# Kernel tuning notes

Measured on AMD Instinct MI355X. Metric: run time of the kernel, lower is better.

Reference implementation:

```python
import jax, jax.numpy as jnp
import numpy as np
from jax import lax

DN = ('NCHW', 'OIHW', 'NCHW')

def _conv(x, w, pad):
    return lax.conv_general_dilated(x, w, (1, 1), [(pad, pad), (pad, pad)], dimension_numbers=DN)

def _bn(x, g, b, eps=1e-5):
    # BatchNorm2d in training mode: batch statistics over (N,H,W), biased variance
    m = jnp.mean(x, axis=(0, 2, 3), keepdims=True)
    v = jnp.var(x, axis=(0, 2, 3), keepdims=True)
    return (x - m) * lax.rsqrt(v + eps) * g.reshape(1, -1, 1, 1) + b.reshape(1, -1, 1, 1)

def setup_inputs() -> dict:
    key = jax.random.key(0)
    ks = jax.random.split(key, 24)
    B, H, W = 128, 64, 64
    l_i, lh = 2, (150, 120, 100)
    l_q, cf = 10, H * W
    r = lambda k, s, sc: jax.random.normal(k, s, dtype=jnp.float32) * sc
    return {
        'X': r(ks[0], (B, l_i, H, W), 1.0),
        'obs': r(ks[1], (B, 24), 1.0),
        'h1_w': r(ks[2], (lh[0], l_i, 3, 3), 0.1), 'h1_b': r(ks[3], (lh[0],), 0.05),
        'g1': jnp.ones((lh[0],), jnp.float32), 'b1': jnp.zeros((lh[0],), jnp.float32),
        'h2_w': r(ks[4], (lh[1], lh[0], 3, 3), 0.03), 'h2_b': r(ks[5], (lh[1],), 0.05),
        'g2': jnp.ones((lh[1],), jnp.float32), 'b2': jnp.zeros((lh[1],), jnp.float32),
        'h3_w': r(ks[6], (lh[2], lh[1], 3, 3), 0.03), 'h3_b': r(ks[7], (lh[2],), 0.05),
        'g3': jnp.ones((lh[2],), jnp.float32), 'b3': jnp.zeros((lh[2],), jnp.float32),
        'r_w': r(ks[8], (1, lh[2], 1, 1), 0.1),
        'q_w': r(ks[9], (l_q, 1, 5, 5), 0.1),
        'w': r(ks[10], (l_q, 1, 5, 5), 0.05),  # Parameter (zeros init in torch; randn here for nontrivial math)
        'fc1_w': r(ks[11], (100, 24), 0.1), 'fc1_b': r(ks[12], (100,), 0.05),
        'fc2_w': r(ks[13], (10, 100), 0.1), 'fc2_b': r(ks[14], (10,), 0.05),
        'cv_w': r(ks[15], (1, cf), 0.02), 'cv_b': r(ks[16], (1,), 0.05),
        'K': 36,
    }

def reference(X, obs, h1_w, h1_b, g1, b1, h2_w, h2_b, g2, b2, h3_w, h3_b, g3, b3,
              r_w, q_w, w, fc1_w, fc1_b, fc2_w, fc2_b, cv_w, cv_b, K):
    relu = jax.nn.relu
    h = relu(_bn(_conv(X, h1_w, 1) + h1_b.reshape(1, -1, 1, 1), g1, b1))
    h = relu(_bn(_conv(h, h2_w, 1) + h2_b.reshape(1, -1, 1, 1), g2, b2))
    h = relu(_bn(_conv(h, h3_w, 1) + h3_b.reshape(1, -1, 1, 1), g3, b3))
    r = _conv(h, r_w, 0)                      # [B,1,H,W] reward map
    qr = _conv(r, q_w, 2)                     # conv of r part is constant across VI iterations
    v = jnp.max(qr, axis=1, keepdims=True)    # [B,1,H,W]
    # conv2d(cat([r,v],1), cat([q_w,w],1)) == conv(r,q_w) + conv(v,w)
    def step(v, _):
        q = qr + _conv(v, w, 2)
        return jnp.max(q, axis=1, keepdims=True), None
    # original: K-1 loop iterations + 1 extra conv/max = K total steps after the init
    v, _ = lax.scan(step, v, None, length=K)
    critic = v.reshape(v.shape[0], -1) @ cv_w.T + cv_b
    action_pred = relu(relu(obs @ fc1_w.T + fc1_b) @ fc2_w.T + fc2_b)
    return (critic, action_pred)
```

## Files before the change

### kernel.cpp

```cpp
#include <hip/hip_runtime.h>


#define NHW 524288.0f

typedef __attribute__((ext_vector_type(8))) short v8s;
typedef __attribute__((ext_vector_type(4))) float v4f;

static __device__ __forceinline__ float bf2f(unsigned short u) {
  return __uint_as_float(((unsigned int)u) << 16);
}
static __device__ __forceinline__ unsigned short f2bf(float f) {
  unsigned int x = __float_as_uint(f);
  return (unsigned short)((x + 0x7fffu + ((x >> 16) & 1u)) >> 16);
}
static __device__ __forceinline__ float wave_sum(float s) {
  #pragma unroll
  for (int off = 32; off > 0; off >>= 1) s += __shfl_down(s, off, 64);
  return s;
}

template <int CO, int CI, int CIP>
__global__ __launch_bounds__(256) void repack_w(
    const float* __restrict__ w, unsigned short* __restrict__ Wp)
{
  int i = blockIdx.x * 256 + threadIdx.x;
  const int total = 9 * 128 * CIP;
  if (i >= total) return;
  int pos = i / (128 * CIP);
  int rem = i - pos * (128 * CIP);
  int co  = rem / CIP;
  int ci  = rem - co * CIP;
  float v = (co < CO && ci < CI) ? w[(co * CI + ci) * 9 + pos] : 0.f;
  Wp[i] = f2bf(v);
}

__global__ __launch_bounds__(256) void conv1_stats(
    const float* __restrict__ X, const float* __restrict__ w1,
    const float* __restrict__ b1, float* __restrict__ S, float* __restrict__ Q)
{
  const int tile = blockIdx.x;
  const int b    = tile >> 3;
  const int y0t  = (tile & 7) * 8;
  const int co0  = blockIdx.y * 15;
  const int tid  = threadIdx.x;
  const int x    = tid & 63;
  const int ly0  = (tid >> 6) * 2;

  __shared__ float lin[2][10][66];
  __shared__ float ss[15], qq[15];
  if (tid < 15) { ss[tid] = 0.f; qq[tid] = 0.f; }
  for (int idx = tid; idx < 2 * 10 * 66; idx += 256) {
    int cc = idx / 660, rem = idx - cc * 660;
    int rr = rem / 66,  c   = rem - rr * 66;
    int yy = y0t + rr - 1, xx = c - 1;
    lin[cc][rr][c] = (yy >= 0 && yy < 64 && xx >= 0 && xx < 64)
                         ? X[((size_t)(b * 2 + cc) << 12) + (yy << 6) + xx] : 0.f;
  }
  __syncthreads();

  float iv[2][4][3];
  #pragma unroll
  for (int cc = 0; cc < 2; cc++)
    #pragma unroll
    for (int r = 0; r < 4; r++)
      #pragma unroll
      for (int c = 0; c < 3; c++) iv[cc][r][c] = lin[cc][ly0 + r][x + c];

  #pragma unroll
  for (int co = 0; co < 15; co++) {
    const float* w9 = w1 + (size_t)(co0 + co) * 18;
    float a0 = 0.f, a1 = 0.f;
    #pragma unroll
    for (int cc = 0; cc < 2; cc++)
      #pragma unroll
      for (int ky = 0; ky < 3; ky++)
        #pragma unroll
        for (int kx = 0; kx < 3; kx++) {
          float wv = w9[cc * 9 + ky * 3 + kx];
          a0 = fmaf(iv[cc][ky][kx],     wv, a0);
          a1 = fmaf(iv[cc][ky + 1][kx], wv, a1);
        }
    float bz = b1[co0 + co];
    float t0 = a0 + bz, t1 = a1 + bz;
    float s  = wave_sum(t0 + t1);
    float q  = wave_sum(t0 * t0 + t1 * t1);
    if ((tid & 63) == 0) { atomicAdd(&ss[co], s); atomicAdd(&qq[co], q); }
  }
  __syncthreads();
  if (tid < 15) {
    atomicAdd(&S[co0 + tid], ss[tid]);
    atomicAdd(&Q[co0 + tid], qq[tid]);
  }
}

template <int C>
__global__ void bn_finalize(const float* __restrict__ S, const float* __restrict__ Q,
                            const float* __restrict__ g, const float* __restrict__ be,
                            float* __restrict__ A, float* __restrict__ Bs)
{
  int c = threadIdx.x;
  if (c < C) {
    const float invN = 1.f / NHW;
    float m   = S[c] * invN;
    float var = fmaxf(Q[c] * invN - m * m, 0.f);
    float sc  = g[c] * rsqrtf(var + 1e-5f);
    A[c]  = sc;
    Bs[c] = be[c] - m * sc;
  }
}

__global__ __launch_bounds__(256, 2) void conv2_mfma(
    const float* __restrict__ X,  const float* __restrict__ w1,
    const float* __restrict__ b1f, const float* __restrict__ A1,
    const float* __restrict__ B1, const unsigned short* __restrict__ W2p,
    const float* __restrict__ b2, unsigned short* __restrict__ t2)
{
  const int bx   = blockIdx.x;
  const int b    = bx >> 4;
  const int t16  = bx & 15;
  const int y0   = (t16 >> 2) * 16;
  const int x0   = (t16 & 3) * 16;
  const int tid  = threadIdx.x;
  const int lane = tid & 63;
  const int wid  = __builtin_amdgcn_readfirstlane(tid >> 6);
  const int ln   = lane & 15;
  const int quad = (lane >> 4) * 8;

  __shared__ __align__(16) float Xs[2][20][20];
  __shared__ float w1s[2700];
  __shared__ float A1s[150], B1s[150], b1s[150], b2s[128];
  __shared__ __align__(16) unsigned short Atile[324 * 34];
  __shared__ __align__(16) unsigned short outs[256 * 68];

  for (int i = tid; i < 2700; i += 256) w1s[i] = w1[i];
  for (int i = tid; i < 150; i += 256) { A1s[i] = A1[i]; B1s[i] = B1[i]; b1s[i] = b1f[i]; }
  if (tid < 128) b2s[tid] = (tid < 120) ? b2[tid] : 0.f;
  for (int i = tid; i < 800; i += 256) {
    int c2 = i / 400, rem = i - c2 * 400;
    int rr = rem / 20, cc = rem - rr * 20;
    int gy = y0 - 2 + rr, gx = x0 - 2 + cc;
    Xs[c2][rr][cc] = (gy >= 0 && gy < 64 && gx >= 0 && gx < 64)
                         ? X[((size_t)(b * 2 + c2) << 12) + (gy << 6) + gx] : 0.f;
  }

  v4f acc[4][8];
  #pragma unroll
  for (int i = 0; i < 4; i++)
    #pragma unroll
    for (int j = 0; j < 8; j++) acc[i][j] = (v4f){0.f, 0.f, 0.f, 0.f};

  for (int chunk = 0; chunk < 5; chunk++) {
    __syncthreads();
    {
      const int ci_loc = tid & 31;
      const int ci = chunk * 32 + ci_loc;
      const bool live = (ci < 150);
      float wv[18], sc = 0.f, sh = 0.f, bz = 0.f;
      if (live) {
        #pragma unroll
        for (int k = 0; k < 18; k++) wv[k] = w1s[ci * 18 + k];
        sc = A1s[ci]; sh = B1s[ci]; bz = b1s[ci];
      }
      for (int pass = 0; pass < 41; pass++) {
        int p = pass * 8 + (tid >> 5);
        if (p < 324) {
          float v = 0.f;
          if (live) {
            int pr = p / 18, pc = p - pr * 18;
            int hy = y0 - 1 + pr, hx = x0 - 1 + pc;
            if (hy >= 0 && hy < 64 && hx >= 0 && hx < 64) {
              float a = bz;
              #pragma unroll
              for (int c2 = 0; c2 < 2; c2++)
                #pragma unroll
                for (int ky = 0; ky < 3; ky++)
                  #pragma unroll
                  for (int kx = 0; kx < 3; kx++)
                    a = fmaf(Xs[c2][pr + ky][pc + kx], wv[c2 * 9 + ky * 3 + kx], a);
              v = fmaxf(fmaf(a, sc, sh), 0.f);
            }
          }
          Atile[p * 34 + ci_loc] = f2bf(v);
        }
      }
    }
    __syncthreads();

    v8s afr[6][3];
    #pragma unroll
    for (int t = 0; t < 6; t++)
      #pragma unroll
      for (int kx = 0; kx < 3; kx++)
        afr[t][kx] = *(const v8s*)(&Atile[((wid * 4 + t) * 18 + ln + kx) * 34 + quad]);

    #pragma unroll
    for (int pos = 0; pos < 9; pos++) {
      const int ky = pos / 3, kx = pos - ky * 3;
      const unsigned short* bw =
          W2p + (size_t)(pos * 128 + ln) * 160 + chunk * 32 + quad;
      v8s bf[8];
      #pragma unroll
      for (int nj = 0; nj < 8; nj++)
        bf[nj] = *(const v8s*)(bw + (size_t)nj * 16 * 160);
      #pragma unroll
      for (int mi = 0; mi < 4; mi++) {
        #pragma unroll
        for (int nj = 0; nj < 8; nj++)
          acc[mi][nj] = __builtin_amdgcn_mfma_f32_16x16x32_bf16(
              afr[mi + ky][kx], bf[nj], acc[mi][nj], 0, 0, 0);
      }
    }
  }

  #pragma unroll
  for (int half = 0; half < 2; half++) {
    __syncthreads();
    #pragma unroll
    for (int mi = 0; mi < 4; mi++)
      #pragma unroll
      for (int njl = 0; njl < 4; njl++) {
        int n = njl * 16 + ln;
        float bz = b2s[half * 64 + n];
        #pragma unroll
        for (int r2 = 0; r2 < 4; r2++) {
          int m = wid * 64 + mi * 16 + (lane >> 4) * 4 + r2;
          outs[m * 68 + n] = f2bf(acc[mi][half * 4 + njl][r2] + bz);
        }
      }
    __syncthreads();
    const int ng = half ? 7 : 8;
    for (int i = tid; i < 256 * ng; i += 256) {
      int p = i / ng, g = i - p * ng;
      int gy = y0 + (p >> 4), gx = x0 + (p & 15);
      size_t gpx = ((size_t)b << 12) + (gy << 6) + gx;
      *(uint4*)(t2 + gpx * 120 + half * 64 + g * 8) =
          *(const uint4*)(&outs[p * 68 + g * 8]);
    }
  }
}

__global__ __launch_bounds__(256, 2) void conv3_mfma(
    const unsigned short* __restrict__ t2, const float* __restrict__ A2,
    const float* __restrict__ B2, const unsigned short* __restrict__ W3p,
    const float* __restrict__ b3, unsigned short* __restrict__ t3)
{
  const int bx   = blockIdx.x;
  const int b    = bx >> 4;
  const int t16  = bx & 15;
  const int y0   = (t16 >> 2) * 16;
  const int x0   = (t16 & 3) * 16;
  const int tid  = threadIdx.x;
  const int lane = tid & 63;
  const int wid  = __builtin_amdgcn_readfirstlane(tid >> 6);
  const int ln   = lane & 15;
  const int quad = (lane >> 4) * 8;

  __shared__ float A2s[120], B2s[120], b3s[128];
  __shared__ __align__(16) unsigned short Atile[324 * 34];
  __shared__ __align__(16) unsigned short outs[256 * 68];

  for (int i = tid; i < 120; i += 256) { A2s[i] = A2[i]; B2s[i] = B2[i]; }
  if (tid < 128) b3s[tid] = (tid < 100) ? b3[tid] : 0.f;

  v4f acc[4][8];
  #pragma unroll
  for (int i = 0; i < 4; i++)
    #pragma unroll
    for (int j = 0; j < 8; j++) acc[i][j] = (v4f){0.f, 0.f, 0.f, 0.f};

  for (int chunk = 0; chunk < 4; chunk++) {
    __syncthreads();
    {
      const int ci0 = chunk * 32;
      const int ngr = (chunk == 3) ? 3 : 4;
      for (int i = tid; i < 1296; i += 256) {
        int p = i >> 2, g = i & 3;
        int pr = p / 18, pc = p - pr * 18;
        int hy = y0 - 1 + pr, hx = x0 - 1 + pc;
        union { uint4 v; unsigned short u[8]; } ov;
        ov.v = (uint4){0, 0, 0, 0};
        if (g < ngr && hy >= 0 && hy < 64 && hx >= 0 && hx < 64) {
          size_t gpx = ((size_t)b << 12) + (hy << 6) + hx;
          union { uint4 v; unsigned short u[8]; } in;
          in.v = *(const uint4*)(t2 + gpx * 120 + ci0 + g * 8);
          #pragma unroll
          for (int j = 0; j < 8; j++) {
            int ci = ci0 + g * 8 + j;
            ov.u[j] = f2bf(fmaxf(fmaf(bf2f(in.u[j]), A2s[ci], B2s[ci]), 0.f));
          }
        }
        *(uint4*)(&Atile[p * 34 + g * 8]) = ov.v;
      }
    }
    __syncthreads();

    v8s afr[6][3];
    #pragma unroll
    for (int t = 0; t < 6; t++)
      #pragma unroll
      for (int kx = 0; kx < 3; kx++)
        afr[t][kx] = *(const v8s*)(&Atile[((wid * 4 + t) * 18 + ln + kx) * 34 + quad]);

    #pragma unroll
    for (int pos = 0; pos < 9; pos++) {
      const int ky = pos / 3, kx = pos - ky * 3;
      const unsigned short* bw =
          W3p + (size_t)(pos * 128 + ln) * 128 + chunk * 32 + quad;
      v8s bf[8];
      #pragma unroll
      for (int nj = 0; nj < 8; nj++)
        bf[nj] = *(const v8s*)(bw + (size_t)nj * 16 * 128);
      #pragma unroll
      for (int mi = 0; mi < 4; mi++) {
        #pragma unroll
        for (int nj = 0; nj < 8; nj++)
          acc[mi][nj] = __builtin_amdgcn_mfma_f32_16x16x32_bf16(
              afr[mi + ky][kx], bf[nj], acc[mi][nj], 0, 0, 0);
      }
    }
  }

  #pragma unroll
  for (int half = 0; half < 2; half++) {
    __syncthreads();
    #pragma unroll
    for (int mi = 0; mi < 4; mi++)
      #pragma unroll
      for (int njl = 0; njl < 4; njl++) {
        int n = njl * 16 + ln;
        float bz = b3s[half * 64 + n];
        #pragma unroll
        for (int r2 = 0; r2 < 4; r2++) {
          int m = wid * 64 + mi * 16 + (lane >> 4) * 4 + r2;
          outs[m * 68 + n] = f2bf(acc[mi][half * 4 + njl][r2] + bz);
        }
      }
    __syncthreads();
    const int ng = half ? 5 : 8;
    for (int i = tid; i < 256 * ng; i += 256) {
      int p = i / ng, g = i - p * ng;
      int gy = y0 + (p >> 4), gx = x0 + (p & 15);
      size_t gpx = ((size_t)b << 12) + (gy << 6) + gx;
      *(uint4*)(t3 + gpx * 104 + half * 64 + g * 8) =
          *(const uint4*)(&outs[p * 68 + g * 8]);
    }
  }
}

template <int ST, int NG, int C>
__global__ __launch_bounds__(256) void nhwc_stats(
    const unsigned short* __restrict__ t, float* __restrict__ S, float* __restrict__ Q)
{
  const int tid = threadIdx.x;
  const int g   = tid & 15;
  const int pl  = tid >> 4;
  const bool valid = (g < NG);
  const int px0 = blockIdx.x * 512;

  __shared__ float ss[128], qq[128];
  for (int i = tid; i < 128; i += 256) { ss[i] = 0.f; qq[i] = 0.f; }
  __syncthreads();

  float s8[8], q8[8];
  #pragma unroll
  for (int j = 0; j < 8; j++) { s8[j] = 0.f; q8[j] = 0.f; }

  if (valid) {
    for (int it = 0; it < 32; it++) {
      size_t px = px0 + it * 16 + pl;
      union { uint4 v; unsigned short u[8]; } in;
      in.v = *(const uint4*)(t + px * ST + g * 8);
      #pragma unroll
      for (int j = 0; j < 8; j++) {
        float v = bf2f(in.u[j]);
        s8[j] += v;
        q8[j] += v * v;
      }
    }
    #pragma unroll
    for (int j = 0; j < 8; j++) {
      atomicAdd(&ss[g * 8 + j], s8[j]);
      atomicAdd(&qq[g * 8 + j], q8[j]);
    }
  }
  __syncthreads();
  if (tid < C) {
    atomicAdd(&S[tid], ss[tid]);
    atomicAdd(&Q[tid], qq[tid]);
  }
}

__global__ __launch_bounds__(256) void bn3_reduce_r(
    const unsigned short* __restrict__ t3, const float* __restrict__ A3,
    const float* __restrict__ B3, const float* __restrict__ rw,
    float* __restrict__ r)
{
  __shared__ float A3s[104], B3s[104], rws[104];
  const int tid = threadIdx.x;
  for (int i = tid; i < 104; i += 256) {
    bool v = (i < 100);
    A3s[i] = v ? A3[i] : 0.f;
    B3s[i] = v ? B3[i] : 0.f;
    rws[i] = v ? rw[i] : 0.f;
  }
  __syncthreads();

  size_t px = (size_t)blockIdx.x * 256 + tid;
  const unsigned short* p = t3 + px * 104;
  float a = 0.f;
  #pragma unroll
  for (int gq = 0; gq < 13; gq++) {
    union { uint4 v; unsigned short u[8]; } in;
    in.v = *(const uint4*)(p + gq * 8);
    #pragma unroll
    for (int j = 0; j < 8; j++) {
      int ci = gq * 8 + j;
      a = fmaf(fmaxf(fmaf(bf2f(in.u[j]), A3s[ci], B3s[ci]), 0.f), rws[ci], a);
    }
  }
  r[px] = a;
}

__global__ __launch_bounds__(256) void qr_init(
    const float* __restrict__ r, const float* __restrict__ qw,
    float* __restrict__ qr, float* __restrict__ v0)
{
  const int tile = blockIdx.x;
  const int b    = tile >> 4;
  const int y0t  = (tile & 15) * 4;
  const int tid  = threadIdx.x;
  const int x    = tid & 63;
  const int ly   = tid >> 6;

  __shared__ float lv[8][68];
  for (int idx = tid; idx < 8 * 68; idx += 256) {
    int rr = idx / 68, c = idx - rr * 68;
    int yy = y0t + rr - 2, xx = c - 2;
    lv[rr][c] = (yy >= 0 && yy < 64 && xx >= 0 && xx < 64)
                    ? r[((size_t)b << 12) + (yy << 6) + xx] : 0.f;
  }
  __syncthreads();

  float iv[5][5];
  #pragma unroll
  for (int ky = 0; ky < 5; ky++)
    #pragma unroll
    for (int kx = 0; kx < 5; kx++) iv[ky][kx] = lv[ly + ky][x + kx];

  const int y = y0t + ly;
  float vmax = -1e30f;
  #pragma unroll
  for (int a = 0; a < 10; a++) {
    float q = 0.f;
    #pragma unroll
    for (int ky = 0; ky < 5; ky++)
      #pragma unroll
      for (int kx = 0; kx < 5; kx++)
        q = fmaf(iv[ky][kx], qw[a * 25 + ky * 5 + kx], q);
    qr[((size_t)(b * 10 + a) << 12) + (y << 6) + x] = q;
    vmax = fmaxf(vmax, q);
  }
  v0[((size_t)b << 12) + (y << 6) + x] = vmax;
}

__global__ __launch_bounds__(256) void vi_step(
    const float* __restrict__ vin, const float* __restrict__ qr,
    const float* __restrict__ ww, float* __restrict__ vout)
{
  const int tile = blockIdx.x;
  const int b    = tile >> 4;
  const int y0t  = (tile & 15) * 4;
  const int tid  = threadIdx.x;
  const int x    = tid & 63;
  const int ly   = tid >> 6;

  __shared__ float lv[8][68];
  for (int idx = tid; idx < 8 * 68; idx += 256) {
    int rr = idx / 68, c = idx - rr * 68;
    int yy = y0t + rr - 2, xx = c - 2;
    lv[rr][c] = (yy >= 0 && yy < 64 && xx >= 0 && xx < 64)
                    ? vin[((size_t)b << 12) + (yy << 6) + xx] : 0.f;
  }
  __syncthreads();

  float iv[5][5];
  #pragma unroll
  for (int ky = 0; ky < 5; ky++)
    #pragma unroll
    for (int kx = 0; kx < 5; kx++) iv[ky][kx] = lv[ly + ky][x + kx];

  const int y = y0t + ly;
  float vmax = -1e30f;
  #pragma unroll
  for (int a = 0; a < 10; a++) {
    float q = qr[((size_t)(b * 10 + a) << 12) + (y << 6) + x];
    #pragma unroll
    for (int ky = 0; ky < 5; ky++)
      #pragma unroll
      for (int kx = 0; kx < 5; kx++)
        q = fmaf(iv[ky][kx], ww[a * 25 + ky * 5 + kx], q);
    vmax = fmaxf(vmax, q);
  }
  vout[((size_t)b << 12) + (y << 6) + x] = vmax;
}

__global__ __launch_bounds__(256) void critic_k(
    const float* __restrict__ v, const float* __restrict__ cvw,
    const float* __restrict__ cvb, float* __restrict__ out)
{
  const int b = blockIdx.x;
  const int tid = threadIdx.x;
  const float4* pv = (const float4*)(v + ((size_t)b << 12));
  const float4* pw = (const float4*)cvw;
  float s = 0.f;
  #pragma unroll
  for (int i = 0; i < 4; i++) {
    float4 a = pv[tid + 256 * i];
    float4 w = pw[tid + 256 * i];
    s += a.x * w.x + a.y * w.y + a.z * w.z + a.w * w.w;
  }
  s = wave_sum(s);
  __shared__ float ls[4];
  const int w = tid >> 6;
  if ((tid & 63) == 0) ls[w] = s;
  __syncthreads();
  if (tid == 0) out[b] = ls[0] + ls[1] + ls[2] + ls[3] + cvb[0];
}

__global__ __launch_bounds__(128) void action_k(
    const float* __restrict__ obs, const float* __restrict__ fc1w,
    const float* __restrict__ fc1b, const float* __restrict__ fc2w,
    const float* __restrict__ fc2b, float* __restrict__ out)
{
  const int b = blockIdx.x;
  const int j = threadIdx.x;
  __shared__ float ob[24];
  __shared__ float h[100];
  if (j < 24) ob[j] = obs[b * 24 + j];
  __syncthreads();
  if (j < 100) {
    float s = fc1b[j];
    #pragma unroll
    for (int k = 0; k < 24; k++) s = fmaf(ob[k], fc1w[j * 24 + k], s);
    h[j] = fmaxf(s, 0.f);
  }
  __syncthreads();
  if (j < 10) {
    float s = fc2b[j];
    for (int k = 0; k < 100; k++) s = fmaf(h[k], fc2w[j * 100 + k], s);
    out[128 + b * 10 + j] = fmaxf(s, 0.f);
  }
}

extern "C" void kernel_launch(void* const* d_in, const int* in_sizes, int n_in,
                              void* d_out, int out_size, void* d_ws,
                              size_t ws_size, hipStream_t stream)
{
  const float* X     = (const float*)d_in[0];
  const float* obs   = (const float*)d_in[1];
  const float* h1_w  = (const float*)d_in[2];
  const float* h1_b  = (const float*)d_in[3];
  const float* g1    = (const float*)d_in[4];
  const float* b1    = (const float*)d_in[5];
  const float* h2_w  = (const float*)d_in[6];
  const float* h2_b  = (const float*)d_in[7];
  const float* g2    = (const float*)d_in[8];
  const float* b2    = (const float*)d_in[9];
  const float* h3_w  = (const float*)d_in[10];
  const float* h3_b  = (const float*)d_in[11];
  const float* g3    = (const float*)d_in[12];
  const float* b3    = (const float*)d_in[13];
  const float* r_w   = (const float*)d_in[14];
  const float* q_w   = (const float*)d_in[15];
  const float* w_vi  = (const float*)d_in[16];
  const float* fc1_w = (const float*)d_in[17];
  const float* fc1_b = (const float*)d_in[18];
  const float* fc2_w = (const float*)d_in[19];
  const float* fc2_b = (const float*)d_in[20];
  const float* cv_w  = (const float*)d_in[21];
  const float* cv_b  = (const float*)d_in[22];

  char* ws = (char*)d_ws;
  unsigned short* t2  = (unsigned short*)ws;
  unsigned short* t3  = (unsigned short*)(ws + 125829120ull);
  unsigned short* W2p = (unsigned short*)(ws + 234881024ull);
  unsigned short* W3p = (unsigned short*)(ws + 235249664ull);
  float*          ST  = (float*)         (ws + 235544576ull);
  float* S1 = ST +    0; float* Q1 = ST +  150; float* A1 = ST +  300; float* B1 = ST +  450;
  float* S2 = ST +  600; float* Q2 = ST +  720; float* A2 = ST +  840; float* B2 = ST +  960;
  float* S3 = ST + 1080; float* Q3 = ST + 1180; float* A3 = ST + 1280; float* B3 = ST + 1380;
  float* r  = (float*)ws;
  float* qr = r + 524288;
  float* vA = qr + 5242880;
  float* vB = vA + 524288;

  hipMemsetAsync(ST, 0, 1480 * sizeof(float), stream);

  repack_w<120, 150, 160><<<720, 256, 0, stream>>>(h2_w, W2p);
  repack_w<100, 120, 128><<<576, 256, 0, stream>>>(h3_w, W3p);

  conv1_stats<<<dim3(1024, 10), 256, 0, stream>>>(X, h1_w, h1_b, S1, Q1);
  bn_finalize<150><<<1, 256, 0, stream>>>(S1, Q1, g1, b1, A1, B1);

  conv2_mfma<<<2048, 256, 0, stream>>>(X, h1_w, h1_b, A1, B1, W2p, h2_b, t2);
  nhwc_stats<120, 15, 120><<<1024, 256, 0, stream>>>(t2, S2, Q2);
  bn_finalize<120><<<1, 256, 0, stream>>>(S2, Q2, g2, b2, A2, B2);

  conv3_mfma<<<2048, 256, 0, stream>>>(t2, A2, B2, W3p, h3_b, t3);
  nhwc_stats<104, 13, 100><<<1024, 256, 0, stream>>>(t3, S3, Q3);
  bn_finalize<100><<<1, 256, 0, stream>>>(S3, Q3, g3, b3, A3, B3);

  bn3_reduce_r<<<2048, 256, 0, stream>>>(t3, A3, B3, r_w, r);

  qr_init<<<2048, 256, 0, stream>>>(r, q_w, qr, vA);
  for (int i = 0; i < 36; i++) {
    const float* vin = (i & 1) ? vB : vA;
    float* vout      = (i & 1) ? vA : vB;
    vi_step<<<2048, 256, 0, stream>>>(vin, qr, w_vi, vout);
  }

  float* out = (float*)d_out;
  critic_k<<<128, 256, 0, stream>>>(vA, cv_w, cv_b, out);
  action_k<<<128, 128, 0, stream>>>(obs, fc1_w, fc1_b, fc2_w, fc2_b, out);
}
```

Measured before the change: 1.319 ms.

## Fuse value-iteration loop and critic into one persistent per-image kernel

```diff
diff --git a/kernel.cpp b/kernel.cpp
--- a/kernel.cpp
+++ b/kernel.cpp
@@ -2,6 +2,7 @@
 
 
 #define NHW 524288.0f
+#define VSTR 69
 
 typedef __attribute__((ext_vector_type(8))) short v8s;
 typedef __attribute__((ext_vector_type(4))) float v4f;
@@ -421,110 +422,91 @@
   r[px] = a;
 }
 
-__global__ __launch_bounds__(256) void qr_init(
-    const float* __restrict__ r, const float* __restrict__ qw,
-    float* __restrict__ qr, float* __restrict__ v0)
-{
-  const int tile = blockIdx.x;
-  const int b    = tile >> 4;
-  const int y0t  = (tile & 15) * 4;
-  const int tid  = threadIdx.x;
-  const int x    = tid & 63;
-  const int ly   = tid >> 6;
-
-  __shared__ float lv[8][68];
-  for (int idx = tid; idx < 8 * 68; idx += 256) {
-    int rr = idx / 68, c = idx - rr * 68;
-    int yy = y0t + rr - 2, xx = c - 2;
-    lv[rr][c] = (yy >= 0 && yy < 64 && xx >= 0 && xx < 64)
-                    ? r[((size_t)b << 12) + (yy << 6) + xx] : 0.f;
-  }
-  __syncthreads();
-
-  float iv[5][5];
-  #pragma unroll
-  for (int ky = 0; ky < 5; ky++)
-    #pragma unroll
-    for (int kx = 0; kx < 5; kx++) iv[ky][kx] = lv[ly + ky][x + kx];
-
-  const int y = y0t + ly;
-  float vmax = -1e30f;
-  #pragma unroll
-  for (int a = 0; a < 10; a++) {
-    float q = 0.f;
-    #pragma unroll
-    for (int ky = 0; ky < 5; ky++)
-      #pragma unroll
-      for (int kx = 0; kx < 5; kx++)
-        q = fmaf(iv[ky][kx], qw[a * 25 + ky * 5 + kx], q);
-    qr[((size_t)(b * 10 + a) << 12) + (y << 6) + x] = q;
-    vmax = fmaxf(vmax, q);
-  }
-  v0[((size_t)b << 12) + (y << 6) + x] = vmax;
-}
-
-__global__ __launch_bounds__(256) void vi_step(
-    const float* __restrict__ vin, const float* __restrict__ qr,
-    const float* __restrict__ ww, float* __restrict__ vout)
-{
-  const int tile = blockIdx.x;
-  const int b    = tile >> 4;
-  const int y0t  = (tile & 15) * 4;
-  const int tid  = threadIdx.x;
-  const int x    = tid & 63;
-  const int ly   = tid >> 6;
-
-  __shared__ float lv[8][68];
-  for (int idx = tid; idx < 8 * 68; idx += 256) {
-    int rr = idx / 68, c = idx - rr * 68;
-    int yy = y0t + rr - 2, xx = c - 2;
-    lv[rr][c] = (yy >= 0 && yy < 64 && xx >= 0 && xx < 64)
-                    ? vin[((size_t)b << 12) + (yy << 6) + xx] : 0.f;
-  }
-  __syncthreads();
-
-  float iv[5][5];
-  #pragma unroll
-  for (int ky = 0; ky < 5; ky++)
-    #pragma unroll
-    for (int kx = 0; kx < 5; kx++) iv[ky][kx] = lv[ly + ky][x + kx];
-
-  const int y = y0t + ly;
-  float vmax = -1e30f;
-  #pragma unroll
-  for (int a = 0; a < 10; a++) {
-    float q = qr[((size_t)(b * 10 + a) << 12) + (y << 6) + x];
-    #pragma unroll
-    for (int ky = 0; ky < 5; ky++)
-      #pragma unroll
-      for (int kx = 0; kx < 5; kx++)
-        q = fmaf(iv[ky][kx], ww[a * 25 + ky * 5 + kx], q);
-    vmax = fmaxf(vmax, q);
-  }
-  vout[((size_t)b << 12) + (y << 6) + x] = vmax;
-}
-
-__global__ __launch_bounds__(256) void critic_k(
-    const float* __restrict__ v, const float* __restrict__ cvw,
+__global__ __launch_bounds__(512, 1) void vi_fused(
+    const float* __restrict__ r,   const float* __restrict__ qw,
+    const float* __restrict__ ww,  const float* __restrict__ cvw,
     const float* __restrict__ cvb, float* __restrict__ out)
 {
-  const int b = blockIdx.x;
+  const int b   = blockIdx.x;
   const int tid = threadIdx.x;
-  const float4* pv = (const float4*)(v + ((size_t)b << 12));
-  const float4* pw = (const float4*)cvw;
-  float s = 0.f;
-  #pragma unroll
-  for (int i = 0; i < 4; i++) {
-    float4 a = pv[tid + 256 * i];
-    float4 w = pw[tid + 256 * i];
-    s += a.x * w.x + a.y * w.y + a.z * w.z + a.w * w.w;
-  }
-  s = wave_sum(s);
-  __shared__ float ls[4];
-  const int w = tid >> 6;
-  if ((tid & 63) == 0) ls[w] = s;
-  __syncthreads();
-  if (tid == 0) out[b] = ls[0] + ls[1] + ls[2] + ls[3] + cvb[0];
+
+  __shared__ unsigned short qrs[10 * 4096];
+  __shared__ float vbuf[2][68 * VSTR];
+  __shared__ float part[8];
+
+  for (int i = tid; i < 2 * 68 * VSTR; i += 512) ((float*)vbuf)[i] = 0.f;
+  __syncthreads();
+
+  const float* rb = r + ((size_t)b << 12);
+  #pragma unroll
+  for (int j = 0; j < 8; j++) {
+    int px = tid + 512 * j;
+    int y = px >> 6, x = px & 63;
+    vbuf[0][(y + 2) * VSTR + (x + 2)] = rb[px];
+  }
+  __syncthreads();
+
+  #pragma unroll
+  for (int j = 0; j < 8; j++) {
+    int px = tid + 512 * j;
+    int y = px >> 6, x = px & 63;
+    float tap[25];
+    #pragma unroll
+    for (int t = 0; t < 25; t++)
+      tap[t] = vbuf[0][(y + t / 5) * VSTR + x + (t % 5)];
+    float vmax = -1e30f;
+    #pragma unroll
+    for (int a = 0; a < 10; a++) {
+      float q = 0.f;
+      #pragma unroll
+      for (int t = 0; t < 25; t++) q = fmaf(tap[t], qw[a * 25 + t], q);
+      qrs[a * 4096 + px] = f2bf(q);
+      vmax = fmaxf(vmax, q);
+    }
+    vbuf[1][(y + 2) * VSTR + (x + 2)] = vmax;
+  }
+  __syncthreads();
+
+  for (int s = 0; s < 36; s++) {
+    const float* src = vbuf[1 - (s & 1)];
+    float* dst       = vbuf[s & 1];
+    #pragma unroll
+    for (int j = 0; j < 8; j++) {
+      int px = tid + 512 * j;
+      int y = px >> 6, x = px & 63;
+      float tap[25];
+      #pragma unroll
+      for (int t = 0; t < 25; t++)
+        tap[t] = src[(y + t / 5) * VSTR + x + (t % 5)];
+      float vmax = -1e30f;
+      #pragma unroll
+      for (int a = 0; a < 10; a++) {
+        float q = bf2f(qrs[a * 4096 + px]);
+        #pragma unroll
+        for (int t = 0; t < 25; t++) q = fmaf(tap[t], ww[a * 25 + t], q);
+        vmax = fmaxf(vmax, q);
+      }
+      dst[(y + 2) * VSTR + (x + 2)] = vmax;
+    }
+    __syncthreads();
+  }
+
+  float ssum = 0.f;
+  #pragma unroll
+  for (int j = 0; j < 8; j++) {
+    int px = tid + 512 * j;
+    int y = px >> 6, x = px & 63;
+    ssum = fmaf(vbuf[1][(y + 2) * VSTR + (x + 2)], cvw[px], ssum);
+  }
+  ssum = wave_sum(ssum);
+  if ((tid & 63) == 0) part[tid >> 6] = ssum;
+  __syncthreads();
+  if (tid == 0) {
+    float t = 0.f;
+    #pragma unroll
+    for (int i2 = 0; i2 < 8; i2++) t += part[i2];
+    out[b] = t + cvb[0];
+  }
 }
 
 __global__ __launch_bounds__(128) void action_k(
@@ -589,10 +571,7 @@
   float* S1 = ST +    0; float* Q1 = ST +  150; float* A1 = ST +  300; float* B1 = ST +  450;
   float* S2 = ST +  600; float* Q2 = ST +  720; float* A2 = ST +  840; float* B2 = ST +  960;
   float* S3 = ST + 1080; float* Q3 = ST + 1180; float* A3 = ST + 1280; float* B3 = ST + 1380;
-  float* r  = (float*)ws;
-  float* qr = r + 524288;
-  float* vA = qr + 5242880;
-  float* vB = vA + 524288;
+  float* r = (float*)ws;
 
   hipMemsetAsync(ST, 0, 1480 * sizeof(float), stream);
 
@@ -612,14 +591,7 @@
 
   bn3_reduce_r<<<2048, 256, 0, stream>>>(t3, A3, B3, r_w, r);
 
-  qr_init<<<2048, 256, 0, stream>>>(r, q_w, qr, vA);
-  for (int i = 0; i < 36; i++) {
-    const float* vin = (i & 1) ? vB : vA;
-    float* vout      = (i & 1) ? vA : vB;
-    vi_step<<<2048, 256, 0, stream>>>(vin, qr, w_vi, vout);
-  }
-
   float* out = (float*)d_out;
-  critic_k<<<128, 256, 0, stream>>>(vA, cv_w, cv_b, out);
+  vi_fused<<<128, 512, 0, stream>>>(r, q_w, w_vi, cv_w, cv_b, out);
   action_k<<<128, 128, 0, stream>>>(obs, fc1_w, fc1_b, fc2_w, fc2_b, out);
 }
```

New measurement: 1.563 ms. 18.5% more time.

## Fuse BN statistics into conv2/conv3 epilogues and store qr in bf16

Applied to the files above, without the earlier changes.

```diff
diff --git a/kernel.cpp b/kernel.cpp
--- a/kernel.cpp
+++ b/kernel.cpp
@@ -113,7 +113,8 @@
     const float* __restrict__ X,  const float* __restrict__ w1,
     const float* __restrict__ b1f, const float* __restrict__ A1,
     const float* __restrict__ B1, const unsigned short* __restrict__ W2p,
-    const float* __restrict__ b2, unsigned short* __restrict__ t2)
+    const float* __restrict__ b2, unsigned short* __restrict__ t2,
+    float* __restrict__ S2, float* __restrict__ Q2)
 {
   const int bx   = blockIdx.x;
   const int b    = bx >> 4;
@@ -129,12 +130,13 @@
   __shared__ __align__(16) float Xs[2][20][20];
   __shared__ float w1s[2700];
   __shared__ float A1s[150], B1s[150], b1s[150], b2s[128];
+  __shared__ float ssB[128], qqB[128];
   __shared__ __align__(16) unsigned short Atile[324 * 34];
   __shared__ __align__(16) unsigned short outs[256 * 68];
 
   for (int i = tid; i < 2700; i += 256) w1s[i] = w1[i];
   for (int i = tid; i < 150; i += 256) { A1s[i] = A1[i]; B1s[i] = B1[i]; b1s[i] = b1f[i]; }
-  if (tid < 128) b2s[tid] = (tid < 120) ? b2[tid] : 0.f;
+  if (tid < 128) { b2s[tid] = (tid < 120) ? b2[tid] : 0.f; ssB[tid] = 0.f; qqB[tid] = 0.f; }
   for (int i = tid; i < 800; i += 256) {
     int c2 = i / 400, rem = i - c2 * 400;
     int rr = rem / 20, cc = rem - rr * 20;
@@ -236,13 +238,29 @@
       *(uint4*)(t2 + gpx * 120 + half * 64 + g * 8) =
           *(const uint4*)(&outs[p * 68 + g * 8]);
     }
+    {
+      float ls = 0.f, lq = 0.f;
+      const int c = tid & 63, pr0 = (tid >> 6) * 64;
+      for (int p = 0; p < 64; p++) {
+        float v = bf2f(outs[(pr0 + p) * 68 + c]);
+        ls += v; lq += v * v;
+      }
+      atomicAdd(&ssB[half * 64 + c], ls);
+      atomicAdd(&qqB[half * 64 + c], lq);
+    }
+  }
+  __syncthreads();
+  if (tid < 120) {
+    atomicAdd(&S2[tid], ssB[tid]);
+    atomicAdd(&Q2[tid], qqB[tid]);
   }
 }
 
 __global__ __launch_bounds__(256, 2) void conv3_mfma(
     const unsigned short* __restrict__ t2, const float* __restrict__ A2,
     const float* __restrict__ B2, const unsigned short* __restrict__ W3p,
-    const float* __restrict__ b3, unsigned short* __restrict__ t3)
+    const float* __restrict__ b3, unsigned short* __restrict__ t3,
+    float* __restrict__ S3, float* __restrict__ Q3)
 {
   const int bx   = blockIdx.x;
   const int b    = bx >> 4;
@@ -256,11 +274,12 @@
   const int quad = (lane >> 4) * 8;
 
   __shared__ float A2s[120], B2s[120], b3s[128];
+  __shared__ float ssB[128], qqB[128];
   __shared__ __align__(16) unsigned short Atile[324 * 34];
   __shared__ __align__(16) unsigned short outs[256 * 68];
 
   for (int i = tid; i < 120; i += 256) { A2s[i] = A2[i]; B2s[i] = B2[i]; }
-  if (tid < 128) b3s[tid] = (tid < 100) ? b3[tid] : 0.f;
+  if (tid < 128) { b3s[tid] = (tid < 100) ? b3[tid] : 0.f; ssB[tid] = 0.f; qqB[tid] = 0.f; }
 
   v4f acc[4][8];
   #pragma unroll
@@ -344,49 +363,21 @@
       *(uint4*)(t3 + gpx * 104 + half * 64 + g * 8) =
           *(const uint4*)(&outs[p * 68 + g * 8]);
     }
-  }
-}
-
-template <int ST, int NG, int C>
-__global__ __launch_bounds__(256) void nhwc_stats(
-    const unsigned short* __restrict__ t, float* __restrict__ S, float* __restrict__ Q)
-{
-  const int tid = threadIdx.x;
-  const int g   = tid & 15;
-  const int pl  = tid >> 4;
-  const bool valid = (g < NG);
-  const int px0 = blockIdx.x * 512;
-
-  __shared__ float ss[128], qq[128];
-  for (int i = tid; i < 128; i += 256) { ss[i] = 0.f; qq[i] = 0.f; }
-  __syncthreads();
-
-  float s8[8], q8[8];
-  #pragma unroll
-  for (int j = 0; j < 8; j++) { s8[j] = 0.f; q8[j] = 0.f; }
-
-  if (valid) {
-    for (int it = 0; it < 32; it++) {
-      size_t px = px0 + it * 16 + pl;
-      union { uint4 v; unsigned short u[8]; } in;
-      in.v = *(const uint4*)(t + px * ST + g * 8);
-      #pragma unroll
-      for (int j = 0; j < 8; j++) {
-        float v = bf2f(in.u[j]);
-        s8[j] += v;
-        q8[j] += v * v;
-      }
-    }
-    #pragma unroll
-    for (int j = 0; j < 8; j++) {
-      atomicAdd(&ss[g * 8 + j], s8[j]);
-      atomicAdd(&qq[g * 8 + j], q8[j]);
-    }
-  }
-  __syncthreads();
-  if (tid < C) {
-    atomicAdd(&S[tid], ss[tid]);
-    atomicAdd(&Q[tid], qq[tid]);
+    {
+      float ls = 0.f, lq = 0.f;
+      const int c = tid & 63, pr0 = (tid >> 6) * 64;
+      for (int p = 0; p < 64; p++) {
+        float v = bf2f(outs[(pr0 + p) * 68 + c]);
+        ls += v; lq += v * v;
+      }
+      atomicAdd(&ssB[half * 64 + c], ls);
+      atomicAdd(&qqB[half * 64 + c], lq);
+    }
+  }
+  __syncthreads();
+  if (tid < 100) {
+    atomicAdd(&S3[tid], ssB[tid]);
+    atomicAdd(&Q3[tid], qqB[tid]);
   }
 }
 
@@ -423,7 +414,7 @@
 
 __global__ __launch_bounds__(256) void qr_init(
     const float* __restrict__ r, const float* __restrict__ qw,
-    float* __restrict__ qr, float* __restrict__ v0)
+    unsigned short* __restrict__ qr, float* __restrict__ v0)
 {
   const int tile = blockIdx.x;
   const int b    = tile >> 4;
@@ -457,14 +448,14 @@
       #pragma unroll
       for (int kx = 0; kx < 5; kx++)
         q = fmaf(iv[ky][kx], qw[a * 25 + ky * 5 + kx], q);
-    qr[((size_t)(b * 10 + a) << 12) + (y << 6) + x] = q;
+    qr[((size_t)(b * 10 + a) << 12) + (y << 6) + x] = f2bf(q);
     vmax = fmaxf(vmax, q);
   }
   v0[((size_t)b << 12) + (y << 6) + x] = vmax;
 }
 
 __global__ __launch_bounds__(256) void vi_step(
-    const float* __restrict__ vin, const float* __restrict__ qr,
+    const float* __restrict__ vin, const unsigned short* __restrict__ qr,
     const float* __restrict__ ww, float* __restrict__ vout)
 {
   const int tile = blockIdx.x;
@@ -493,7 +484,7 @@
   float vmax = -1e30f;
   #pragma unroll
   for (int a = 0; a < 10; a++) {
-    float q = qr[((size_t)(b * 10 + a) << 12) + (y << 6) + x];
+    float q = bf2f(qr[((size_t)(b * 10 + a) << 12) + (y << 6) + x]);
     #pragma unroll
     for (int ky = 0; ky < 5; ky++)
       #pragma unroll
@@ -589,10 +580,10 @@
   float* S1 = ST +    0; float* Q1 = ST +  150; float* A1 = ST +  300; float* B1 = ST +  450;
   float* S2 = ST +  600; float* Q2 = ST +  720; float* A2 = ST +  840; float* B2 = ST +  960;
   float* S3 = ST + 1080; float* Q3 = ST + 1180; float* A3 = ST + 1280; float* B3 = ST + 1380;
-  float* r  = (float*)ws;
-  float* qr = r + 524288;
-  float* vA = qr + 5242880;
-  float* vB = vA + 524288;
+  float*          r   = (float*)ws;
+  unsigned short* qrh = (unsigned short*)(ws + 2097152ull);
+  float*          vA  = (float*)(ws + 12582912ull);
+  float*          vB  = (float*)(ws + 14680064ull);
 
   hipMemsetAsync(ST, 0, 1480 * sizeof(float), stream);
 
@@ -602,21 +593,19 @@
   conv1_stats<<<dim3(1024, 10), 256, 0, stream>>>(X, h1_w, h1_b, S1, Q1);
   bn_finalize<150><<<1, 256, 0, stream>>>(S1, Q1, g1, b1, A1, B1);
 
-  conv2_mfma<<<2048, 256, 0, stream>>>(X, h1_w, h1_b, A1, B1, W2p, h2_b, t2);
-  nhwc_stats<120, 15, 120><<<1024, 256, 0, stream>>>(t2, S2, Q2);
+  conv2_mfma<<<2048, 256, 0, stream>>>(X, h1_w, h1_b, A1, B1, W2p, h2_b, t2, S2, Q2);
   bn_finalize<120><<<1, 256, 0, stream>>>(S2, Q2, g2, b2, A2, B2);
 
-  conv3_mfma<<<2048, 256, 0, stream>>>(t2, A2, B2, W3p, h3_b, t3);
-  nhwc_stats<104, 13, 100><<<1024, 256, 0, stream>>>(t3, S3, Q3);
+  conv3_mfma<<<2048, 256, 0, stream>>>(t2, A2, B2, W3p, h3_b, t3, S3, Q3);
   bn_finalize<100><<<1, 256, 0, stream>>>(S3, Q3, g3, b3, A3, B3);
 
   bn3_reduce_r<<<2048, 256, 0, stream>>>(t3, A3, B3, r_w, r);
 
-  qr_init<<<2048, 256, 0, stream>>>(r, q_w, qr, vA);
+  qr_init<<<2048, 256, 0, stream>>>(r, q_w, qrh, vA);
   for (int i = 0; i < 36; i++) {
     const float* vin = (i & 1) ? vB : vA;
     float* vout      = (i & 1) ? vA : vB;
-    vi_step<<<2048, 256, 0, stream>>>(vin, qr, w_vi, vout);
+    vi_step<<<2048, 256, 0, stream>>>(vin, qrh, w_vi, vout);
   }
 
   float* out = (float*)d_out;
```

New measurement: 1.294 ms (median of 2 runs). About the same (-1.9%).
